# Optimization experiments

Measured on AMD Instinct MI355X. Metric: run time of the kernel, lower is better.

The kernel has to match this reference:

```python
import jax, jax.numpy as jnp
import numpy as np

# LIF neuron constants (standard mem_update)
THRESH = 0.5
LENS = 0.5
DECAY = 0.25
EPS = 1e-5
NUM_HEADS = 8

@jax.custom_vjp
def act_fun(mem):
    return (mem > THRESH).astype(mem.dtype)

def _act_fwd(mem):
    return act_fun(mem), mem

def _act_bwd(mem, g):
    surrogate = (jnp.abs(mem - THRESH) < LENS).astype(g.dtype)
    return (g * surrogate,)

act_fun.defvjp(_act_fwd, _act_bwd)

def mem_update(x):
    # x: (T, ...) -> binary spikes (T, ...) via recurrent LIF dynamics
    def step(carry, xt):
        mem_old, spike = carry
        # spike is detached in the reset gate (torch .detach())
        mem = mem_old * DECAY * (1.0 - jax.lax.stop_gradient(spike)) + xt
        s = act_fun(mem)
        return (mem, s), s
    init = (jnp.zeros_like(x[0]), jnp.zeros_like(x[0]))
    _, out = jax.lax.scan(step, init, x)
    return out

def bn(x, gamma, beta, mean, var):
    # inference-mode BatchNorm1d over channel dim of (T,B,C,L)
    inv = gamma / jnp.sqrt(var + EPS)
    return x * inv[None, None, :, None] + (beta - mean * inv)[None, None, :, None]

def setup_inputs() -> dict:
    key = jax.random.key(0)
    ks = jax.random.split(key, 11)
    T, B, C, L = 4, 2, 384, 1024
    s = 1.0 / np.sqrt(C)
    return {
        "x": jax.random.normal(ks[0], (T, B, C, L), jnp.float32),
        "W_w": jax.random.normal(ks[1], (2 * C, C), jnp.float32) * s,
        "bn1_gamma": jax.random.uniform(ks[2], (2 * C,), jnp.float32, 0.5, 1.5),
        "bn1_beta": jax.random.normal(ks[3], (2 * C,), jnp.float32) * 0.1,
        "bn1_mean": jax.random.normal(ks[4], (2 * C,), jnp.float32) * 0.1,
        "bn1_var": jax.random.uniform(ks[5], (2 * C,), jnp.float32, 0.5, 1.5),
        "proj_w": jax.random.normal(ks[6], (C, C), jnp.float32) * s,
        "bn2_gamma": jax.random.uniform(ks[7], (C,), jnp.float32, 0.5, 1.5),
        "bn2_beta": jax.random.normal(ks[8], (C,), jnp.float32) * 0.1,
        "bn2_mean": jax.random.normal(ks[9], (C,), jnp.float32) * 0.1,
        "bn2_var": jax.random.uniform(ks[10], (C,), jnp.float32, 0.5, 1.5),
    }

def reference(x, W_w, bn1_gamma, bn1_beta, bn1_mean, bn1_var, proj_w, bn2_gamma, bn2_beta, bn2_mean, bn2_var):
    T, B, C, L = x.shape
    H = NUM_HEADS
    d = C // H
    x_feat = x
    xs = mem_update(x)                                   # binary spikes (T,B,C,L)
    y = jnp.einsum('oc,tbcl->tbol', W_w, xs)             # 1x1 conv C->2C
    y = bn(y, bn1_gamma, bn1_beta, bn1_mean, bn1_var)
    y = y.reshape(T, B, H, 2 * d, L)
    y1, y2 = y[:, :, :, :d, :], y[:, :, :, d:, :]
    xr = xs.reshape(T, B, H, d, L)
    attn = jnp.einsum('tbhdl,tbhdm->tbhlm', y1, xr)      # (L,L) per head
    attn = mem_update(attn)                              # binary spikes
    out = jnp.einsum('tbhdl,tbhlm->tbhdm', y2, attn)
    out = out.reshape(T, B, C, L)
    out = mem_update(out)
    out = jnp.einsum('oc,tbcl->tbol', proj_w, out)       # Wproj 1x1
    out = bn(out, bn2_gamma, bn2_beta, bn2_mean, bn2_var)
    return out + x_feat
```

## Files before the change

### kernel.cpp

```cpp
#include <hip/hip_runtime.h>

#define T_  4
#define B_  2
#define C_  384
#define L_  1024
#define H_  8
#define C2_ 768
#define S_  (B_*C_*L_)

typedef __attribute__((ext_vector_type(8))) short short8;
typedef __attribute__((ext_vector_type(4))) float floatx4;
typedef __attribute__((ext_vector_type(16))) float floatx16;

__device__ __forceinline__ unsigned bf16_rne(float v) {
    unsigned u = __float_as_uint(v);
    u += 0x7FFFu + ((u >> 16) & 1u);
    return u >> 16;
}
__device__ __forceinline__ float bf16_to_f(unsigned h) { return __uint_as_float(h << 16); }
__device__ __forceinline__ void split3(float v, unsigned& hi, unsigned& mi, unsigned& lo) {
    hi = bf16_rne(v);
    float r1 = v - bf16_to_f(hi);
    mi = bf16_rne(r1);
    float r2 = r1 - bf16_to_f(mi);
    lo = bf16_rne(r2);
}

__global__ __launch_bounds__(256) void split_w2(
    const float* __restrict__ Wa, int n4a,
    unsigned short* __restrict__ hia, unsigned short* __restrict__ mia,
    unsigned short* __restrict__ loa,
    const float* __restrict__ Wb, int n4b,
    unsigned short* __restrict__ hib, unsigned short* __restrict__ mib,
    unsigned short* __restrict__ lob) {
    int i = blockIdx.x * 256 + threadIdx.x;
    const float* W; unsigned short *hi, *mi, *lo;
    if (i < n4a) { W = Wa; hi = hia; mi = mia; lo = loa; }
    else {
        i -= n4a;
        if (i >= n4b) return;
        W = Wb; hi = hib; mi = mib; lo = lob;
    }
    float4 v = ((const float4*)W)[i];
    float vv[4] = {v.x, v.y, v.z, v.w};
    union { unsigned short us[4]; uint2 u2; } h, m, l;
#pragma unroll
    for (int e = 0; e < 4; e++) {
        unsigned hh, mm, ll; split3(vv[e], hh, mm, ll);
        h.us[e] = (unsigned short)hh; m.us[e] = (unsigned short)mm; l.us[e] = (unsigned short)ll;
    }
    ((uint2*)hi)[i] = h.u2; ((uint2*)mi)[i] = m.u2; ((uint2*)lo)[i] = l.u2;
}

__global__ __launch_bounds__(256) void scan_transpose(const float* __restrict__ src,
                                                      unsigned short* __restrict__ dstT) {
    __shared__ unsigned short tile[64][72];
    const int tid = threadIdx.x;
    const int l0 = blockIdx.x * 64, c0 = blockIdx.y * 64, b = blockIdx.z;
    const int row = tid >> 2, seg = tid & 3;
    float mem[16], sp[16];
#pragma unroll
    for (int e = 0; e < 16; e++) { mem[e] = 0.f; sp[e] = 0.f; }
    for (int t = 0; t < T_; t++) {
        const size_t base = ((size_t)((t*B_ + b)*C_ + c0 + row))*L_ + l0 + seg*16;
#pragma unroll
        for (int qq = 0; qq < 4; qq++) {
            float4 v = *(const float4*)(src + base + qq*4);
            float vv[4] = {v.x, v.y, v.z, v.w};
            unsigned bs[4];
#pragma unroll
            for (int s = 0; s < 4; s++) {
                int e = qq*4 + s;
                mem[e] = mem[e]*0.25f*(1.f - sp[e]) + vv[s];
                bool sb = mem[e] > 0.5f;
                sp[e] = sb ? 1.f : 0.f;
                bs[s] = sb ? 0x3F80u : 0u;
            }
            *(unsigned*)&tile[row][seg*16 + qq*4]     = bs[0] | (bs[1] << 16);
            *(unsigned*)&tile[row][seg*16 + qq*4 + 2] = bs[2] | (bs[3] << 16);
        }
        __syncthreads();
        {
            const int lr = tid >> 2, cs = tid & 3;
#pragma unroll
            for (int sub = 0; sub < 2; sub++) {
                unsigned wv[4];
#pragma unroll
                for (int p = 0; p < 4; p++) {
                    unsigned e0 = tile[cs*16 + sub*8 + p*2][lr];
                    unsigned e1 = tile[cs*16 + sub*8 + p*2 + 1][lr];
                    wv[p] = e0 | (e1 << 16);
                }
                uint4 o; o.x = wv[0]; o.y = wv[1]; o.z = wv[2]; o.w = wv[3];
                *(uint4*)(dstT + ((size_t)(t*B_ + b)*L_ + l0 + lr)*C_ + c0 + cs*16 + sub*8) = o;
            }
        }
        __syncthreads();
    }
}

__global__ __launch_bounds__(256) void gemm1_mfma(
    const unsigned short* __restrict__ whi, const unsigned short* __restrict__ wmi,
    const unsigned short* __restrict__ wlo, const unsigned short* __restrict__ xsT,
    const float* __restrict__ g, const float* __restrict__ be,
    const float* __restrict__ mn, const float* __restrict__ vr,
    unsigned short* __restrict__ y1hi, unsigned short* __restrict__ y1mi,
    unsigned short* __restrict__ y1lo,
    unsigned short* __restrict__ y2hi, unsigned short* __restrict__ y2mi,
    unsigned short* __restrict__ y2lo) {
    __shared__ unsigned short smem[14080];
    const int tid = threadIdx.x;
    const int flat = blockIdx.x;
    const int tb = flat & 7;
    const int ii = flat >> 3;
    const int mt = ii >> 4, lt = ii & 15;
    const int l0 = lt * 64;
    const int w = tid >> 6, lane = tid & 63;
    const int q = lane >> 4, n15 = lane & 15;
    const int mw = (w & 1) * 48, lw = (w >> 1) * 32;

    floatx4 acc[3][2];
#pragma unroll
    for (int i = 0; i < 3; i++)
#pragma unroll
        for (int j = 0; j < 2; j++) acc[i][j] = (floatx4){0.f,0.f,0.f,0.f};

    for (int ck = 0; ck < C_; ck += 32) {
#pragma unroll
        for (int p = 0; p < 3; p++) {
            const unsigned short* wp = p == 0 ? whi : p == 1 ? wmi : wlo;
            unsigned short* ap = smem + p*3840;
            for (int s = tid; s < 384; s += 256) {
                int r = s >> 2, c = s & 3;
                *(uint4*)&ap[r*40 + c*8] = *(const uint4*)(wp + (size_t)(mt*96 + r)*C_ + ck + c*8);
            }
        }
        {
            int r = tid >> 2, c = tid & 3;
            *(uint4*)&smem[11520 + r*40 + c*8] =
                *(const uint4*)(xsT + ((size_t)tb*L_ + l0 + r)*C_ + ck + c*8);
        }
        __syncthreads();
        short8 bb[2];
#pragma unroll
        for (int in = 0; in < 2; in++)
            bb[in] = *(short8*)&smem[11520 + (lw + in*16 + n15)*40 + q*8];
#pragma unroll
        for (int im = 0; im < 3; im++) {
            short8 ah = *(short8*)&smem[       (mw + im*16 + n15)*40 + q*8];
            short8 am = *(short8*)&smem[3840 + (mw + im*16 + n15)*40 + q*8];
            short8 al = *(short8*)&smem[7680 + (mw + im*16 + n15)*40 + q*8];
#pragma unroll
            for (int in = 0; in < 2; in++) {
                acc[im][in] = __builtin_amdgcn_mfma_f32_16x16x32_bf16(ah, bb[in], acc[im][in], 0,0,0);
                acc[im][in] = __builtin_amdgcn_mfma_f32_16x16x32_bf16(am, bb[in], acc[im][in], 0,0,0);
                acc[im][in] = __builtin_amdgcn_mfma_f32_16x16x32_bf16(al, bb[in], acc[im][in], 0,0,0);
            }
        }
        __syncthreads();
    }

#pragma unroll
    for (int im = 0; im < 3; im++)
#pragma unroll
        for (int r = 0; r < 4; r++) {
            int o = mt*96 + mw + im*16 + q*4 + r;
            float inv = g[o] / sqrtf(vr[o] + 1e-5f);
            float sh = be[o] - mn[o]*inv;
#pragma unroll
            for (int in = 0; in < 2; in++)
                acc[im][in][r] = acc[im][in][r]*inv + sh;
        }
    const bool isY1 = ((w & 1) == 0);
#pragma unroll
    for (int p = 0; p < 3; p++) {
        if (isY1) {
#pragma unroll
            for (int im = 0; im < 3; im++)
#pragma unroll
                for (int in = 0; in < 2; in++) {
                    union { unsigned short us[4]; uint2 u2; } pk;
#pragma unroll
                    for (int r = 0; r < 4; r++) {
                        unsigned hh = bf16_rne(acc[im][in][r]);
                        pk.us[r] = (unsigned short)hh;
                        acc[im][in][r] -= bf16_to_f(hh);
                    }
                    *(uint2*)&smem[(lw + in*16 + n15)*56 + im*16 + q*4] = pk.u2;
                }
        } else {
#pragma unroll
            for (int im = 0; im < 3; im++)
#pragma unroll
                for (int in = 0; in < 2; in++)
#pragma unroll
                    for (int r = 0; r < 4; r++) {
                        unsigned hh = bf16_rne(acc[im][in][r]);
                        smem[3584 + (im*16 + q*4 + r)*72 + lw + in*16 + n15] = (unsigned short)hh;
                        acc[im][in][r] -= bf16_to_f(hh);
                    }
        }
        __syncthreads();
        unsigned short* y1p = p == 0 ? y1hi : p == 1 ? y1mi : y1lo;
        unsigned short* y2p = p == 0 ? y2hi : p == 1 ? y2mi : y2lo;
        for (int s = tid; s < 384; s += 256) {
            int r1 = s / 6, c8 = s % 6;
            *(uint4*)(y1p + (((size_t)tb*H_ + mt)*L_ + l0 + r1)*48 + c8*8) =
                *(uint4*)&smem[r1*56 + c8*8];
        }
        for (int s = tid; s < 384; s += 256) {
            int cr = s >> 3, lq = s & 7;
            *(uint4*)(y2p + ((size_t)tb*C_ + mt*48 + cr)*L_ + l0 + lq*8) =
                *(uint4*)&smem[3584 + cr*72 + lq*8];
        }
        __syncthreads();
    }
}

__global__ __launch_bounds__(256) void attn_spike_mfma(
    const unsigned short* __restrict__ y1hi, const unsigned short* __restrict__ y1mi,
    const unsigned short* __restrict__ y1lo, const unsigned short* __restrict__ xsT,
    unsigned* __restrict__ bits) {
    __shared__ unsigned short A_hi[64][56], A_mi[64][56], A_lo[64][56], B_s[64][56];
    __shared__ unsigned bits_s[64][2];
    const int tid = threadIdx.x;
    const int flat = blockIdx.x;
    const int xcd = flat & 7;
    const int ii = flat >> 3;
    const int bh = xcd*2 + (ii >> 8);
    const int rr = ii & 255;
    const int b = bh >> 3, h = bh & 7;
    const int lbase = (rr >> 4)*64, mbase = (rr & 15)*64;
    const int w = tid >> 6, lane = tid & 63;
    const int l31 = lane & 31, half = lane >> 5;
    const int i = w & 1, j = w >> 1;

    float mem[16];
#pragma unroll
    for (int r = 0; r < 16; r++) mem[r] = 0.f;

    for (int t = 0; t < T_; t++) {
        const int tb = t*B_ + b;
        const size_t yb = (((size_t)tb*H_ + h)*L_ + lbase)*48;
        const size_t xb = ((size_t)tb*L_ + mbase)*C_ + h*48;
        for (int s = tid; s < 384; s += 256) {
            int r = s / 6, c = s % 6;
            size_t ro = yb + (size_t)r*48 + c*8;
            *(uint4*)&A_hi[r][c*8] = *(const uint4*)(y1hi + ro);
            *(uint4*)&A_mi[r][c*8] = *(const uint4*)(y1mi + ro);
            *(uint4*)&A_lo[r][c*8] = *(const uint4*)(y1lo + ro);
            *(uint4*)&B_s[r][c*8]  = *(const uint4*)(xsT + xb + (size_t)r*C_ + c*8);
        }
        if (tid < 128) bits_s[tid >> 1][tid & 1] = 0u;
        __syncthreads();

        floatx16 acc = {0.f,0.f,0.f,0.f,0.f,0.f,0.f,0.f,0.f,0.f,0.f,0.f,0.f,0.f,0.f,0.f};
#pragma unroll
        for (int ks = 0; ks < 3; ks++) {
            const int kcol = ks*16 + half*8;
            short8 bb = *(short8*)&B_s[j*32 + l31][kcol];
            short8 ah = *(short8*)&A_hi[i*32 + l31][kcol];
            short8 am = *(short8*)&A_mi[i*32 + l31][kcol];
            short8 al = *(short8*)&A_lo[i*32 + l31][kcol];
            acc = __builtin_amdgcn_mfma_f32_32x32x16_bf16(ah, bb, acc, 0,0,0);
            acc = __builtin_amdgcn_mfma_f32_32x32x16_bf16(am, bb, acc, 0,0,0);
            acc = __builtin_amdgcn_mfma_f32_32x32x16_bf16(al, bb, acc, 0,0,0);
        }

        unsigned word = 0;
#pragma unroll
        for (int r = 0; r < 16; r++) {
            float m = (mem[r] > 0.5f ? 0.f : mem[r]*0.25f) + acc[r];
            mem[r] = m;
            int lloc = (r & 3) + 8*(r >> 2) + 4*half;
            word |= (m > 0.5f) ? (1u << lloc) : 0u;
        }
        atomicOr(&bits_s[j*32 + l31][i], word);
        __syncthreads();
        if (tid < 128) {
            int m = tid >> 1, wd = tid & 1;
            bits[((size_t)(tb*H_ + h)*L_ + mbase + m)*32 + (lbase >> 5) + wd] = bits_s[m][wd];
        }
        __syncthreads();
    }
}

__global__ __launch_bounds__(256) void attn_out_mfma(
    const unsigned short* __restrict__ y2hi, const unsigned short* __restrict__ y2mi,
    const unsigned short* __restrict__ y2lo,
    const unsigned* __restrict__ bits, float* __restrict__ outpre) {
    __shared__ unsigned short A_hi[48][72], A_mi[48][72], A_lo[48][72];
    const int tid = threadIdx.x;
    const int flat = blockIdx.x;
    const int xcd = flat & 7;
    const int ii = flat >> 3;
    const int tbh = xcd*8 + (ii >> 4);
    const int mtile = ii & 15;
    const int t = tbh >> 4, b = (tbh >> 3) & 1, h = tbh & 7;
    const int tb = t*B_ + b;
    const int w = tid >> 6, lane = tid & 63;
    const int q = lane >> 4, n15 = lane & 15;
    const int mb = mtile*64 + w*16;

    floatx4 acc[3];
#pragma unroll
    for (int i = 0; i < 3; i++) acc[i] = (floatx4){0.f,0.f,0.f,0.f};

    const unsigned* brow = bits + ((size_t)(tb*H_ + h)*L_ + mb + n15)*32;
    const size_t y2b = ((size_t)tb*C_ + h*48)*L_;

    for (int lt = 0; lt < L_; lt += 64) {
        for (int s = tid; s < 384; s += 256) {
            int r = s >> 3, c = s & 7;
            size_t ro = y2b + (size_t)r*L_ + lt + c*8;
            *(uint4*)&A_hi[r][c*8] = *(const uint4*)(y2hi + ro);
            *(uint4*)&A_mi[r][c*8] = *(const uint4*)(y2mi + ro);
            *(uint4*)&A_lo[r][c*8] = *(const uint4*)(y2lo + ro);
        }
        uint2 bw = *(const uint2*)(brow + (lt >> 5));
        __syncthreads();
#pragma unroll
        for (int kc = 0; kc < 2; kc++) {
            unsigned word = kc ? bw.y : bw.x;
            unsigned byt = (word >> (q*8)) & 0xFFu;
            union { unsigned u[4]; short8 v; } bu;
#pragma unroll
            for (int p = 0; p < 4; p++)
                bu.u[p] = (((byt >> (2*p)) & 1u) ? 0x3F80u : 0u)
                        | (((byt >> (2*p+1)) & 1u) ? 0x3F800000u : 0u);
            short8 bfrag = bu.v;
#pragma unroll
            for (int i = 0; i < 3; i++) {
                int ra = i*16 + n15;
                short8 ah = *(short8*)&A_hi[ra][kc*32 + q*8];
                short8 am = *(short8*)&A_mi[ra][kc*32 + q*8];
                short8 al = *(short8*)&A_lo[ra][kc*32 + q*8];
                acc[i] = __builtin_amdgcn_mfma_f32_16x16x32_bf16(ah, bfrag, acc[i], 0,0,0);
                acc[i] = __builtin_amdgcn_mfma_f32_16x16x32_bf16(am, bfrag, acc[i], 0,0,0);
                acc[i] = __builtin_amdgcn_mfma_f32_16x16x32_bf16(al, bfrag, acc[i], 0,0,0);
            }
        }
        __syncthreads();
    }
#pragma unroll
    for (int i = 0; i < 3; i++)
#pragma unroll
        for (int r = 0; r < 4; r++) {
            int d = i*16 + q*4 + r;
            outpre[((size_t)tb*C_ + h*48 + d)*L_ + mb + n15] = acc[i][r];
        }
}

__global__ __launch_bounds__(256) void gemm2_mfma(
    const unsigned short* __restrict__ whi, const unsigned short* __restrict__ wmi,
    const unsigned short* __restrict__ wlo, const unsigned short* __restrict__ xT,
    const float* __restrict__ g, const float* __restrict__ be,
    const float* __restrict__ mn, const float* __restrict__ vr,
    const float* __restrict__ res, float* __restrict__ out) {
    __shared__ unsigned short A_hi[96][40], A_mi[96][40], A_lo[96][40];
    __shared__ unsigned short B_s[64][40];
    const int tid = threadIdx.x;
    const int tb = blockIdx.y;
    const int mt = blockIdx.x >> 4, lt = blockIdx.x & 15;
    const int l0 = lt * 64;
    const int w = tid >> 6, lane = tid & 63;
    const int q = lane >> 4, n15 = lane & 15;
    const int mw = (w & 1) * 48, lw = (w >> 1) * 32;

    floatx4 acc[3][2];
#pragma unroll
    for (int i = 0; i < 3; i++)
#pragma unroll
        for (int j = 0; j < 2; j++) acc[i][j] = (floatx4){0.f,0.f,0.f,0.f};

    for (int ck = 0; ck < C_; ck += 32) {
#pragma unroll
        for (int p = 0; p < 3; p++) {
            const unsigned short* wp = p == 0 ? whi : p == 1 ? wmi : wlo;
            unsigned short (*ap)[40] = p == 0 ? A_hi : p == 1 ? A_mi : A_lo;
            for (int s = tid; s < 384; s += 256) {
                int r = s >> 2, c = s & 3;
                *(uint4*)&ap[r][c*8] = *(const uint4*)(wp + (size_t)(mt*96 + r)*C_ + ck + c*8);
            }
        }
        {
            int r = tid >> 2, c4 = tid & 3;
            *(uint4*)&B_s[r][c4*8] = *(const uint4*)(xT + ((size_t)tb*L_ + l0 + r)*C_ + ck + c4*8);
        }
        __syncthreads();
        short8 bb[2];
#pragma unroll
        for (int in = 0; in < 2; in++)
            bb[in] = *(short8*)&B_s[lw + in*16 + n15][q*8];
#pragma unroll
        for (int im = 0; im < 3; im++) {
            short8 ah = *(short8*)&A_hi[mw + im*16 + n15][q*8];
            short8 am = *(short8*)&A_mi[mw + im*16 + n15][q*8];
            short8 al = *(short8*)&A_lo[mw + im*16 + n15][q*8];
#pragma unroll
            for (int in = 0; in < 2; in++) {
                acc[im][in] = __builtin_amdgcn_mfma_f32_16x16x32_bf16(ah, bb[in], acc[im][in], 0,0,0);
                acc[im][in] = __builtin_amdgcn_mfma_f32_16x16x32_bf16(am, bb[in], acc[im][in], 0,0,0);
                acc[im][in] = __builtin_amdgcn_mfma_f32_16x16x32_bf16(al, bb[in], acc[im][in], 0,0,0);
            }
        }
        __syncthreads();
    }
#pragma unroll
    for (int im = 0; im < 3; im++)
#pragma unroll
        for (int r = 0; r < 4; r++) {
            int o = mt*96 + mw + im*16 + q*4 + r;
            float inv = g[o] / sqrtf(vr[o] + 1e-5f);
            float sh = be[o] - mn[o]*inv;
#pragma unroll
            for (int in = 0; in < 2; in++) {
                int l = l0 + lw + in*16 + n15;
                size_t idx = ((size_t)tb*C_ + o)*L_ + l;
                out[idx] = acc[im][in][r]*inv + sh + res[idx];
            }
        }
}

extern "C" void kernel_launch(void* const* d_in, const int* in_sizes, int n_in,
                              void* d_out, int out_size, void* d_ws, size_t ws_size,
                              hipStream_t stream) {
    const float* x   = (const float*)d_in[0];
    const float* W_w = (const float*)d_in[1];
    const float* g1  = (const float*)d_in[2];
    const float* b1  = (const float*)d_in[3];
    const float* m1  = (const float*)d_in[4];
    const float* v1  = (const float*)d_in[5];
    const float* pw  = (const float*)d_in[6];
    const float* g2  = (const float*)d_in[7];
    const float* b2  = (const float*)d_in[8];
    const float* m2  = (const float*)d_in[9];
    const float* v2  = (const float*)d_in[10];

    float* ws = (float*)d_ws;
    unsigned short* xsT  = (unsigned short*)ws;
    unsigned short* y1hi = (unsigned short*)(ws + 1572864);
    unsigned short* y1mi = (unsigned short*)(ws + 3145728);
    unsigned short* y1lo = (unsigned short*)(ws + 4718592);
    unsigned short* y2hi = (unsigned short*)(ws + 6291456);
    unsigned short* y2mi = (unsigned short*)(ws + 7864320);
    unsigned short* y2lo = (unsigned short*)(ws + 9437184);
    unsigned*       bits = (unsigned*)(ws + 11010048);
    unsigned short* wspl[3]  = {(unsigned short*)(ws + 13107200),
                                (unsigned short*)(ws + 13254656),
                                (unsigned short*)(ws + 13402112)};
    unsigned short* pwspl[3] = {(unsigned short*)(ws + 13549568),
                                (unsigned short*)(ws + 13623296),
                                (unsigned short*)(ws + 13697024)};
    float*          outpre = (float*)(ws + 1572864);
    unsigned short* outsT  = (unsigned short*)(ws + 4718592);
    float* out = (float*)d_out;

    split_w2<<<dim3(432), 256, 0, stream>>>(W_w, C2_*C_/4, wspl[0], wspl[1], wspl[2],
                                            pw,  C_*C_/4, pwspl[0], pwspl[1], pwspl[2]);
    scan_transpose<<<dim3(16, 6, B_), 256, 0, stream>>>(x, xsT);
    gemm1_mfma<<<dim3(1024), 256, 0, stream>>>(wspl[0], wspl[1], wspl[2], xsT,
                                               g1, b1, m1, v1,
                                               y1hi, y1mi, y1lo, y2hi, y2mi, y2lo);
    attn_spike_mfma<<<dim3(4096), 256, 0, stream>>>(y1hi, y1mi, y1lo, xsT, bits);
    attn_out_mfma<<<dim3(1024), 256, 0, stream>>>(y2hi, y2mi, y2lo, bits, outpre);
    scan_transpose<<<dim3(16, 6, B_), 256, 0, stream>>>(outpre, outsT);
    gemm2_mfma<<<dim3(64, 8), 256, 0, stream>>>(pwspl[0], pwspl[1], pwspl[2], outsT,
                                                g2, b2, m2, v2, x, out);
}
```

Measured before the change: 220.4 us.

## Double per-block M tile in attention spike and output kernels for operand reuse

The attention-spike kernel now covers 128 m-columns per block instead of 64. Each warp owns a 32-column strip and computes two 32x32 l-subtiles, so the split A fragments are loaded once per block and reused across twice as many columns. The attention-output kernel likewise gives each warp 32 m-columns using two bit-fragment operands against the same A loads. Grids are halved to match. This cuts redundant y1/y2 loads and per-block overhead, at the cost of more registers per thread, which may lower occupancy, and fewer blocks in flight.

```diff
diff --git a/kernel.cpp b/kernel.cpp
--- a/kernel.cpp
+++ b/kernel.cpp
@@ -221,23 +221,25 @@
     const unsigned short* __restrict__ y1hi, const unsigned short* __restrict__ y1mi,
     const unsigned short* __restrict__ y1lo, const unsigned short* __restrict__ xsT,
     unsigned* __restrict__ bits) {
-    __shared__ unsigned short A_hi[64][56], A_mi[64][56], A_lo[64][56], B_s[64][56];
-    __shared__ unsigned bits_s[64][2];
+    __shared__ unsigned short A_hi[64][56], A_mi[64][56], A_lo[64][56], B_s[128][56];
+    __shared__ unsigned bits_s[128][2];
     const int tid = threadIdx.x;
     const int flat = blockIdx.x;
     const int xcd = flat & 7;
     const int ii = flat >> 3;
-    const int bh = xcd*2 + (ii >> 8);
-    const int rr = ii & 255;
+    const int bh = xcd*2 + (ii >> 7);
+    const int rr = ii & 127;
     const int b = bh >> 3, h = bh & 7;
-    const int lbase = (rr >> 4)*64, mbase = (rr & 15)*64;
+    const int lbase = (rr >> 3) * 64;
+    const int mbase = (rr & 7) * 128;
     const int w = tid >> 6, lane = tid & 63;
     const int l31 = lane & 31, half = lane >> 5;
-    const int i = w & 1, j = w >> 1;
-
-    float mem[16];
-#pragma unroll
-    for (int r = 0; r < 16; r++) mem[r] = 0.f;
+
+    float mem[2][16];
+#pragma unroll
+    for (int il = 0; il < 2; il++)
+#pragma unroll
+        for (int r = 0; r < 16; r++) mem[il][r] = 0.f;
 
     for (int t = 0; t < T_; t++) {
         const int tb = t*B_ + b;
@@ -249,35 +251,49 @@
             *(uint4*)&A_hi[r][c*8] = *(const uint4*)(y1hi + ro);
             *(uint4*)&A_mi[r][c*8] = *(const uint4*)(y1mi + ro);
             *(uint4*)&A_lo[r][c*8] = *(const uint4*)(y1lo + ro);
-            *(uint4*)&B_s[r][c*8]  = *(const uint4*)(xsT + xb + (size_t)r*C_ + c*8);
-        }
-        if (tid < 128) bits_s[tid >> 1][tid & 1] = 0u;
-        __syncthreads();
-
-        floatx16 acc = {0.f,0.f,0.f,0.f,0.f,0.f,0.f,0.f,0.f,0.f,0.f,0.f,0.f,0.f,0.f,0.f};
+        }
+        for (int s = tid; s < 768; s += 256) {
+            int r = s / 6, c = s % 6;
+            *(uint4*)&B_s[r][c*8] = *(const uint4*)(xsT + xb + (size_t)r*C_ + c*8);
+        }
+        bits_s[tid >> 1][tid & 1] = 0u;
+        __syncthreads();
+
+        floatx16 acc[2];
+#pragma unroll
+        for (int il = 0; il < 2; il++)
+#pragma unroll
+            for (int r = 0; r < 16; r++) acc[il][r] = 0.f;
+
 #pragma unroll
         for (int ks = 0; ks < 3; ks++) {
             const int kcol = ks*16 + half*8;
-            short8 bb = *(short8*)&B_s[j*32 + l31][kcol];
-            short8 ah = *(short8*)&A_hi[i*32 + l31][kcol];
-            short8 am = *(short8*)&A_mi[i*32 + l31][kcol];
-            short8 al = *(short8*)&A_lo[i*32 + l31][kcol];
-            acc = __builtin_amdgcn_mfma_f32_32x32x16_bf16(ah, bb, acc, 0,0,0);
-            acc = __builtin_amdgcn_mfma_f32_32x32x16_bf16(am, bb, acc, 0,0,0);
-            acc = __builtin_amdgcn_mfma_f32_32x32x16_bf16(al, bb, acc, 0,0,0);
-        }
-
-        unsigned word = 0;
-#pragma unroll
-        for (int r = 0; r < 16; r++) {
-            float m = (mem[r] > 0.5f ? 0.f : mem[r]*0.25f) + acc[r];
-            mem[r] = m;
-            int lloc = (r & 3) + 8*(r >> 2) + 4*half;
-            word |= (m > 0.5f) ? (1u << lloc) : 0u;
-        }
-        atomicOr(&bits_s[j*32 + l31][i], word);
-        __syncthreads();
-        if (tid < 128) {
+            short8 bb = *(short8*)&B_s[w*32 + l31][kcol];
+#pragma unroll
+            for (int il = 0; il < 2; il++) {
+                short8 ah = *(short8*)&A_hi[il*32 + l31][kcol];
+                short8 am = *(short8*)&A_mi[il*32 + l31][kcol];
+                short8 al = *(short8*)&A_lo[il*32 + l31][kcol];
+                acc[il] = __builtin_amdgcn_mfma_f32_32x32x16_bf16(ah, bb, acc[il], 0,0,0);
+                acc[il] = __builtin_amdgcn_mfma_f32_32x32x16_bf16(am, bb, acc[il], 0,0,0);
+                acc[il] = __builtin_amdgcn_mfma_f32_32x32x16_bf16(al, bb, acc[il], 0,0,0);
+            }
+        }
+
+#pragma unroll
+        for (int il = 0; il < 2; il++) {
+            unsigned word = 0;
+#pragma unroll
+            for (int r = 0; r < 16; r++) {
+                float m = (mem[il][r] > 0.5f ? 0.f : mem[il][r]*0.25f) + acc[il][r];
+                mem[il][r] = m;
+                int lloc = (r & 3) + 8*(r >> 2) + 4*half;
+                word |= (m > 0.5f) ? (1u << lloc) : 0u;
+            }
+            atomicOr(&bits_s[w*32 + l31][il], word);
+        }
+        __syncthreads();
+        {
             int m = tid >> 1, wd = tid & 1;
             bits[((size_t)(tb*H_ + h)*L_ + mbase + m)*32 + (lbase >> 5) + wd] = bits_s[m][wd];
         }
@@ -294,19 +310,22 @@
     const int flat = blockIdx.x;
     const int xcd = flat & 7;
     const int ii = flat >> 3;
-    const int tbh = xcd*8 + (ii >> 4);
-    const int mtile = ii & 15;
+    const int tbh = xcd*8 + (ii >> 3);
+    const int mtile = ii & 7;
     const int t = tbh >> 4, b = (tbh >> 3) & 1, h = tbh & 7;
     const int tb = t*B_ + b;
     const int w = tid >> 6, lane = tid & 63;
     const int q = lane >> 4, n15 = lane & 15;
-    const int mb = mtile*64 + w*16;
-
-    floatx4 acc[3];
-#pragma unroll
-    for (int i = 0; i < 3; i++) acc[i] = (floatx4){0.f,0.f,0.f,0.f};
-
-    const unsigned* brow = bits + ((size_t)(tb*H_ + h)*L_ + mb + n15)*32;
+    const int mb = mtile*128 + w*32;
+
+    floatx4 acc[3][2];
+#pragma unroll
+    for (int i = 0; i < 3; i++)
+#pragma unroll
+        for (int in = 0; in < 2; in++) acc[i][in] = (floatx4){0.f,0.f,0.f,0.f};
+
+    const unsigned* brow0 = bits + ((size_t)(tb*H_ + h)*L_ + mb + n15)*32;
+    const unsigned* brow1 = brow0 + 16*32;
     const size_t y2b = ((size_t)tb*C_ + h*48)*L_;
 
     for (int lt = 0; lt < L_; lt += 64) {
@@ -317,27 +336,36 @@
             *(uint4*)&A_mi[r][c*8] = *(const uint4*)(y2mi + ro);
             *(uint4*)&A_lo[r][c*8] = *(const uint4*)(y2lo + ro);
         }
-        uint2 bw = *(const uint2*)(brow + (lt >> 5));
+        uint2 bw0 = *(const uint2*)(brow0 + (lt >> 5));
+        uint2 bw1 = *(const uint2*)(brow1 + (lt >> 5));
         __syncthreads();
 #pragma unroll
         for (int kc = 0; kc < 2; kc++) {
-            unsigned word = kc ? bw.y : bw.x;
-            unsigned byt = (word >> (q*8)) & 0xFFu;
-            union { unsigned u[4]; short8 v; } bu;
-#pragma unroll
-            for (int p = 0; p < 4; p++)
-                bu.u[p] = (((byt >> (2*p)) & 1u) ? 0x3F80u : 0u)
-                        | (((byt >> (2*p+1)) & 1u) ? 0x3F800000u : 0u);
-            short8 bfrag = bu.v;
+            unsigned word0 = kc ? bw0.y : bw0.x;
+            unsigned word1 = kc ? bw1.y : bw1.x;
+            unsigned byt0 = (word0 >> (q*8)) & 0xFFu;
+            unsigned byt1 = (word1 >> (q*8)) & 0xFFu;
+            union { unsigned u[4]; short8 v; } bu0, bu1;
+#pragma unroll
+            for (int p = 0; p < 4; p++) {
+                bu0.u[p] = (((byt0 >> (2*p)) & 1u) ? 0x3F80u : 0u)
+                         | (((byt0 >> (2*p+1)) & 1u) ? 0x3F800000u : 0u);
+                bu1.u[p] = (((byt1 >> (2*p)) & 1u) ? 0x3F80u : 0u)
+                         | (((byt1 >> (2*p+1)) & 1u) ? 0x3F800000u : 0u);
+            }
+            short8 bf0 = bu0.v, bf1 = bu1.v;
 #pragma unroll
             for (int i = 0; i < 3; i++) {
                 int ra = i*16 + n15;
                 short8 ah = *(short8*)&A_hi[ra][kc*32 + q*8];
                 short8 am = *(short8*)&A_mi[ra][kc*32 + q*8];
                 short8 al = *(short8*)&A_lo[ra][kc*32 + q*8];
-                acc[i] = __builtin_amdgcn_mfma_f32_16x16x32_bf16(ah, bfrag, acc[i], 0,0,0);
-                acc[i] = __builtin_amdgcn_mfma_f32_16x16x32_bf16(am, bfrag, acc[i], 0,0,0);
-                acc[i] = __builtin_amdgcn_mfma_f32_16x16x32_bf16(al, bfrag, acc[i], 0,0,0);
+                acc[i][0] = __builtin_amdgcn_mfma_f32_16x16x32_bf16(ah, bf0, acc[i][0], 0,0,0);
+                acc[i][0] = __builtin_amdgcn_mfma_f32_16x16x32_bf16(am, bf0, acc[i][0], 0,0,0);
+                acc[i][0] = __builtin_amdgcn_mfma_f32_16x16x32_bf16(al, bf0, acc[i][0], 0,0,0);
+                acc[i][1] = __builtin_amdgcn_mfma_f32_16x16x32_bf16(ah, bf1, acc[i][1], 0,0,0);
+                acc[i][1] = __builtin_amdgcn_mfma_f32_16x16x32_bf16(am, bf1, acc[i][1], 0,0,0);
+                acc[i][1] = __builtin_amdgcn_mfma_f32_16x16x32_bf16(al, bf1, acc[i][1], 0,0,0);
             }
         }
         __syncthreads();
@@ -347,7 +375,9 @@
 #pragma unroll
         for (int r = 0; r < 4; r++) {
             int d = i*16 + q*4 + r;
-            outpre[((size_t)tb*C_ + h*48 + d)*L_ + mb + n15] = acc[i][r];
+#pragma unroll
+            for (int in = 0; in < 2; in++)
+                outpre[((size_t)tb*C_ + h*48 + d)*L_ + mb + in*16 + n15] = acc[i][in][r];
         }
 }
 
@@ -462,8 +492,8 @@
     gemm1_mfma<<<dim3(1024), 256, 0, stream>>>(wspl[0], wspl[1], wspl[2], xsT,
                                                g1, b1, m1, v1,
                                                y1hi, y1mi, y1lo, y2hi, y2mi, y2lo);
-    attn_spike_mfma<<<dim3(4096), 256, 0, stream>>>(y1hi, y1mi, y1lo, xsT, bits);
-    attn_out_mfma<<<dim3(1024), 256, 0, stream>>>(y2hi, y2mi, y2lo, bits, outpre);
+    attn_spike_mfma<<<dim3(2048), 256, 0, stream>>>(y1hi, y1mi, y1lo, xsT, bits);
+    attn_out_mfma<<<dim3(512), 256, 0, stream>>>(y2hi, y2mi, y2lo, bits, outpre);
     scan_transpose<<<dim3(16, 6, B_), 256, 0, stream>>>(outpre, outsT);
     gemm2_mfma<<<dim3(64, 8), 256, 0, stream>>>(pwspl[0], pwspl[1], pwspl[2], outsT,
                                                 g2, b2, m2, v2, x, out);
```

Result: no change. 222.2 us (+0.8%).
